# Optimization experiments

Measured on AMD Instinct MI355X. Metric: run time of the kernel, lower is better.

The kernel has to match this reference:

```python
import jax, jax.numpy as jnp
import numpy as np

B, C, H, W = 4, 512, 64, 64
INTER = 64  # C // channel_stride


def setup_inputs() -> dict:
    key = jax.random.key(0)
    ks = jax.random.split(key, 5)
    s = 0.02  # small init scale for numerical stability of softmax logits
    return {
        "inputs": jax.random.normal(ks[0], (B, C, H, W), dtype=jnp.float32),
        "Wq": jax.random.normal(ks[1], (INTER, C), dtype=jnp.float32) * s,
        "bq": jnp.zeros((INTER,), dtype=jnp.float32),
        "Wk": jax.random.normal(ks[2], (INTER, C), dtype=jnp.float32) * s,
        "bk": jnp.zeros((INTER,), dtype=jnp.float32),
        "Wv": jax.random.normal(ks[3], (C, C), dtype=jnp.float32) * s,
        "bv": jnp.zeros((C,), dtype=jnp.float32),
        "gamma": jax.random.normal(ks[4], (1,), dtype=jnp.float32),
    }


def reference(inputs, Wq, bq, Wk, bk, Wv, bv, gamma):
    b, c, h, w = inputs.shape
    n = h * w
    x = inputs.reshape(b, c, n)  # (B, C, N)
    # 1x1 convs == per-pixel linear projections
    q = jnp.einsum('dc,bcn->bnd', Wq, x) + bq            # (B, N, d)
    k = jnp.einsum('dc,bcn->bdn', Wk, x) + bk[:, None]   # (B, d, N)
    v = jnp.einsum('oc,bcn->bon', Wv, x) + bv[:, None]   # (B, O, N)
    # affinity: (B, Nq, Nk), softmax over keys (last dim), no scaling (as in source)
    affinity = jax.nn.softmax(jnp.einsum('bnd,bdm->bnm', q, k), axis=-1)
    # note: torch does bmm(value, affinity) -> out[b,o,m] = sum_j v[b,o,j] * A[b,j,m]
    out = jnp.einsum('bon,bnm->bom', v, affinity)        # (B, O, N)
    return gamma * out.reshape(b, -1, h, w) + inputs
```

## Files before the change

### kernel.cpp

```cpp
#include <hip/hip_runtime.h>
#include <stdint.h>

typedef __attribute__((ext_vector_type(8))) short short8;
typedef __attribute__((ext_vector_type(4))) float f32x4;
typedef __attribute__((ext_vector_type(8))) unsigned short u16x8;
typedef __attribute__((ext_vector_type(4))) unsigned short u16x4;
typedef __attribute__((ext_vector_type(2))) unsigned short u16x2;
typedef unsigned short u16;

#define NPIX 4096
#define CCH  512
#define DD   64

__device__ inline float b2f(u16 h){
  union { unsigned int i; float f; } u; u.i = ((unsigned int)h) << 16; return u.f;
}
__device__ inline u16 f2b(float f){
  union { float f; unsigned int i; } u; u.f = f;
  return (u16)((u.i + 0x7fffu + ((u.i >> 16) & 1u)) >> 16);
}
__device__ inline void gl2lds16(const void* g, void* l){
  __builtin_amdgcn_global_load_lds((const __attribute__((address_space(1))) unsigned int*)g,
                                   (__attribute__((address_space(3))) unsigned int*)l, 16, 0, 0);
}
__device__ inline f32x4 mfma16(short8 a, short8 b, f32x4 c){
  return __builtin_amdgcn_mfma_f32_16x16x32_bf16(a, b, c, 0, 0, 0);
}

__global__ __launch_bounds__(256) void k_cvt(const float* __restrict__ src,
                                             u16* __restrict__ dst, int n){
  int i = blockIdx.x * 256 + threadIdx.x;
  if (i < n) dst[i] = f2b(src[i]);
}

__global__ __launch_bounds__(256) void k0_transpose(const float* __restrict__ x,
                                                    u16* __restrict__ xT){
  __shared__ u16 tile[64][66];
  const int b = blockIdx.z;
  const int n0 = blockIdx.x * 64, c0 = blockIdx.y * 64;
  const float* xb = x + ((size_t)b * CCH + c0) * NPIX + n0;
  #pragma unroll
  for (int r = 0; r < 16; ++r){
    int id = r * 256 + threadIdx.x;
    int cc = id >> 6, nn = id & 63;
    tile[nn][cc] = f2b(xb[(size_t)cc * NPIX + nn]);
  }
  __syncthreads();
  u16* xTb = xT + ((size_t)b * NPIX + n0) * CCH + c0;
  #pragma unroll
  for (int r = 0; r < 8; ++r){
    int id = r * 256 + threadIdx.x;
    int nn = id >> 5, c2 = id & 31;
    *(u16x2*)(xTb + (size_t)nn * CCH + 2 * c2) = *(const u16x2*)&tile[nn][2 * c2];
  }
}

__global__ __launch_bounds__(256) void k1_qk(const u16* __restrict__ xT,
    const u16* __restrict__ Wqk, const float* __restrict__ bq,
    const float* __restrict__ bk, u16* __restrict__ Qb, u16* __restrict__ Kb){
  __shared__ __align__(16) u16 As[128*64];
  __shared__ __align__(16) u16 Bs[128*64];
  const int b  = blockIdx.z;
  const int n0 = blockIdx.x * 128;
  const u16* Ab = xT + ((size_t)b * NPIX + n0) * CCH;
  const int t = threadIdx.x, wave = t >> 6, lane = t & 63, q = lane >> 4, l16 = lane & 15;
  const int wr = (wave >> 1) * 64, wc = (wave & 1) * 64;
  f32x4 acc[4][4];
  #pragma unroll
  for (int i = 0; i < 4; ++i)
    #pragma unroll
    for (int j = 0; j < 4; ++j) acc[i][j] = (f32x4){0.f,0.f,0.f,0.f};

  for (int k0 = 0; k0 < CCH; k0 += 64){
    __syncthreads();
    #pragma unroll
    for (int r = 0; r < 4; ++r){
      int id = r * 256 + t;
      int row = id >> 3, ko = (id & 7) << 3;
      gl2lds16(Ab + (size_t)row * CCH + k0 + ko, &As[id * 8]);
      gl2lds16(Wqk + (size_t)row * CCH + k0 + ko, &Bs[id * 8]);
    }
    __syncthreads();
    #pragma unroll
    for (int s = 0; s < 2; ++s){
      short8 af[4], bfr[4];
      #pragma unroll
      for (int i = 0; i < 4; ++i){
        af[i]  = *(const short8*)&As[(wr + i*16 + l16)*64 + s*32 + q*8];
        bfr[i] = *(const short8*)&Bs[(wc + i*16 + l16)*64 + s*32 + q*8];
      }
      #pragma unroll
      for (int i = 0; i < 4; ++i)
        #pragma unroll
        for (int j = 0; j < 4; ++j)
          acc[i][j] = mfma16(af[i], bfr[j], acc[i][j]);
    }
  }
  #pragma unroll
  for (int i = 0; i < 4; ++i){
    #pragma unroll
    for (int j = 0; j < 4; ++j){
      int col = wc + j*16 + l16;
      #pragma unroll
      for (int r2 = 0; r2 < 4; ++r2){
        int n = n0 + wr + i*16 + q*4 + r2;
        float v = acc[i][j][r2];
        if (col < 64) Qb[((size_t)b * NPIX + n) * DD + col]        = f2b(v + bq[col]);
        else          Kb[((size_t)b * NPIX + n) * DD + (col - 64)] = f2b(v + bk[col - 64]);
      }
    }
  }
}

__global__ __launch_bounds__(256) void k2_v(const u16* __restrict__ xT,
    const u16* __restrict__ Wvb, const float* __restrict__ bv, u16* __restrict__ Vb){
  __shared__ __align__(16) u16 As[128*64];
  __shared__ __align__(16) u16 Bs[128*64];
  const int b  = blockIdx.z;
  const int n0 = blockIdx.x * 128;
  const int o0 = blockIdx.y * 128;
  const u16* Ab = Wvb + (size_t)o0 * CCH;
  const u16* Bb = xT + ((size_t)b * NPIX + n0) * CCH;
  const int t = threadIdx.x, wave = t >> 6, lane = t & 63, q = lane >> 4, l16 = lane & 15;
  const int wr = (wave >> 1) * 64, wc = (wave & 1) * 64;
  f32x4 acc[4][4];
  #pragma unroll
  for (int i = 0; i < 4; ++i)
    #pragma unroll
    for (int j = 0; j < 4; ++j) acc[i][j] = (f32x4){0.f,0.f,0.f,0.f};

  for (int k0 = 0; k0 < CCH; k0 += 64){
    __syncthreads();
    #pragma unroll
    for (int r = 0; r < 4; ++r){
      int id = r * 256 + t;
      int row = id >> 3, ko = (id & 7) << 3;
      gl2lds16(Ab + (size_t)row * CCH + k0 + ko, &As[id * 8]);
      gl2lds16(Bb + (size_t)row * CCH + k0 + ko, &Bs[id * 8]);
    }
    __syncthreads();
    #pragma unroll
    for (int s = 0; s < 2; ++s){
      short8 af[4], bfr[4];
      #pragma unroll
      for (int i = 0; i < 4; ++i){
        af[i]  = *(const short8*)&As[(wr + i*16 + l16)*64 + s*32 + q*8];
        bfr[i] = *(const short8*)&Bs[(wc + i*16 + l16)*64 + s*32 + q*8];
      }
      #pragma unroll
      for (int i = 0; i < 4; ++i)
        #pragma unroll
        for (int j = 0; j < 4; ++j)
          acc[i][j] = mfma16(af[i], bfr[j], acc[i][j]);
    }
  }
  #pragma unroll
  for (int i = 0; i < 4; ++i){
    #pragma unroll
    for (int j = 0; j < 4; ++j){
      int n = n0 + wc + j*16 + l16;
      #pragma unroll
      for (int r2 = 0; r2 < 4; ++r2){
        int o = o0 + wr + i*16 + q*4 + r2;
        Vb[((size_t)b * CCH + o) * NPIX + n] = f2b(acc[i][j][r2] + bv[o]);
      }
    }
  }
}

__global__ __launch_bounds__(256) void k3_logits(const u16* __restrict__ Qb,
    const u16* __restrict__ Kb, u16* __restrict__ E, float* __restrict__ Z, int b0){
  __shared__ __align__(16) u16 smem[128*136];
  u16* As = smem;
  u16* Bs = smem + 128*64;
  const int bloc = blockIdx.z, b = b0 + bloc;
  const int n0 = blockIdx.x * 128;
  const int m0 = blockIdx.y * 128;
  const u16* Ab = Kb + ((size_t)b * NPIX + m0) * DD;
  const u16* Bb = Qb + ((size_t)b * NPIX + n0) * DD;
  const int t = threadIdx.x, wave = t >> 6, lane = t & 63, q = lane >> 4, l16 = lane & 15;
  const int wr = (wave >> 1) * 64, wc = (wave & 1) * 64;
  f32x4 acc[4][4];
  #pragma unroll
  for (int i = 0; i < 4; ++i)
    #pragma unroll
    for (int j = 0; j < 4; ++j) acc[i][j] = (f32x4){0.f,0.f,0.f,0.f};

  #pragma unroll
  for (int r = 0; r < 4; ++r){
    int id = r * 256 + t;
    int row = id >> 3, ko = (id & 7) << 3;
    gl2lds16(Ab + row * DD + ko, &As[id * 8]);
    gl2lds16(Bb + row * DD + ko, &Bs[id * 8]);
  }
  __syncthreads();
  #pragma unroll
  for (int s = 0; s < 2; ++s){
    short8 af[4], bfr[4];
    #pragma unroll
    for (int i = 0; i < 4; ++i){
      af[i]  = *(const short8*)&As[(wr + i*16 + l16)*64 + s*32 + q*8];
      bfr[i] = *(const short8*)&Bs[(wc + i*16 + l16)*64 + s*32 + q*8];
    }
    #pragma unroll
    for (int i = 0; i < 4; ++i)
      #pragma unroll
      for (int j = 0; j < 4; ++j)
        acc[i][j] = mfma16(af[i], bfr[j], acc[i][j]);
  }
  __syncthreads();
  u16* tile = smem;
  float colsum[4] = {0.f, 0.f, 0.f, 0.f};
  #pragma unroll
  for (int i = 0; i < 4; ++i){
    #pragma unroll
    for (int j = 0; j < 4; ++j){
      #pragma unroll
      for (int r2 = 0; r2 < 4; ++r2){
        int mrow = wr + i*16 + q*4 + r2;
        int ncol = wc + j*16 + l16;
        float l = fminf(fmaxf(acc[i][j][r2], -60.f), 30.f);
        float e = __expf(l);
        tile[mrow * 136 + ncol] = f2b(e);
        colsum[j] += e;
      }
    }
  }
  #pragma unroll
  for (int j = 0; j < 4; ++j){
    float v = colsum[j];
    v += __shfl_xor(v, 16, 64);
    v += __shfl_xor(v, 32, 64);
    if (q == 0) atomicAdd(&Z[(size_t)b * NPIX + n0 + wc + j*16 + l16], v);
  }
  __syncthreads();
  u16* Eb = E + (size_t)bloc * NPIX * NPIX;
  #pragma unroll
  for (int r = 0; r < 8; ++r){
    int id = r * 256 + t;
    int row = id >> 4, chunk = id & 15;
    *(u16x8*)(Eb + (size_t)(m0 + row) * NPIX + n0 + chunk * 8) =
        *(const u16x8*)&tile[row * 136 + chunk * 8];
  }
}

__global__ __launch_bounds__(256) void k3b_scale(u16* __restrict__ Vb,
    const float* __restrict__ Z, const float* __restrict__ gm, int b0){
  size_t i4  = ((size_t)blockIdx.x * 256 + threadIdx.x) * 4;
  size_t off = ((size_t)b0 << 21) + i4;
  int b = (int)(off >> 21);
  int n = (int)(off & (NPIX - 1));
  float g = gm[0];
  u16x4 vv = *(const u16x4*)(Vb + off);
  f32x4 zz = *(const f32x4*)(Z + ((size_t)b << 12) + n);
  u16x4 r;
  #pragma unroll
  for (int k = 0; k < 4; ++k) r[k] = f2b(g * b2f(vv[k]) / fmaxf(zz[k], 1e-20f));
  *(u16x4*)(Vb + off) = r;
}

__global__ __launch_bounds__(256) void k4_out(const u16* __restrict__ Vs,
    const u16* __restrict__ E, const float* __restrict__ xin,
    float* __restrict__ outp, int b0){
  __shared__ __align__(16) u16 As[128*64];
  __shared__ __align__(16) u16 Bs[128*64];
  const int bloc = blockIdx.z, b = b0 + bloc;
  const int m0 = blockIdx.x * 128;
  const int o0 = blockIdx.y * 128;
  const u16* Ab = Vs + ((size_t)b * CCH + o0) * NPIX;
  const u16* Bb = E + (size_t)bloc * NPIX * NPIX + (size_t)m0 * NPIX;
  const int t = threadIdx.x, wave = t >> 6, lane = t & 63, q = lane >> 4, l16 = lane & 15;
  const int wr = (wave >> 1) * 64, wc = (wave & 1) * 64;
  f32x4 acc[4][4];
  #pragma unroll
  for (int i = 0; i < 4; ++i)
    #pragma unroll
    for (int j = 0; j < 4; ++j) acc[i][j] = (f32x4){0.f,0.f,0.f,0.f};

  for (int k0 = 0; k0 < NPIX; k0 += 64){
    __syncthreads();
    #pragma unroll
    for (int r = 0; r < 4; ++r){
      int id = r * 256 + t;
      int row = id >> 3, ko = (id & 7) << 3;
      gl2lds16(Ab + (size_t)row * NPIX + k0 + ko, &As[id * 8]);
      gl2lds16(Bb + (size_t)row * NPIX + k0 + ko, &Bs[id * 8]);
    }
    __syncthreads();
    #pragma unroll
    for (int s = 0; s < 2; ++s){
      short8 af[4], bfr[4];
      #pragma unroll
      for (int i = 0; i < 4; ++i){
        af[i]  = *(const short8*)&As[(wr + i*16 + l16)*64 + s*32 + q*8];
        bfr[i] = *(const short8*)&Bs[(wc + i*16 + l16)*64 + s*32 + q*8];
      }
      #pragma unroll
      for (int i = 0; i < 4; ++i)
        #pragma unroll
        for (int j = 0; j < 4; ++j)
          acc[i][j] = mfma16(af[i], bfr[j], acc[i][j]);
    }
  }
  const float* xb = xin + (size_t)b * CCH * NPIX;
  float* ob = outp + (size_t)b * CCH * NPIX;
  #pragma unroll
  for (int i = 0; i < 4; ++i){
    #pragma unroll
    for (int j = 0; j < 4; ++j){
      int m = m0 + wc + j*16 + l16;
      #pragma unroll
      for (int r2 = 0; r2 < 4; ++r2){
        int o = o0 + wr + i*16 + q*4 + r2;
        size_t idx = (size_t)o * NPIX + m;
        ob[idx] = acc[i][j][r2] + xb[idx];
      }
    }
  }
}

extern "C" void kernel_launch(void* const* d_in, const int* in_sizes, int n_in,
                              void* d_out, int out_size, void* d_ws, size_t ws_size,
                              hipStream_t stream){
  (void)in_sizes; (void)n_in; (void)out_size;
  const float* x  = (const float*)d_in[0];
  const float* Wq = (const float*)d_in[1];
  const float* bq = (const float*)d_in[2];
  const float* Wk = (const float*)d_in[3];
  const float* bk = (const float*)d_in[4];
  const float* Wv = (const float*)d_in[5];
  const float* bv = (const float*)d_in[6];
  const float* gm = (const float*)d_in[7];
  float* outp = (float*)d_out;

  char* ws = (char*)d_ws;
  u16*  Qb   = (u16*)(ws + 0);
  u16*  Kb   = (u16*)(ws + 2097152);
  u16*  Vb   = (u16*)(ws + 4194304);
  float* Z   = (float*)(ws + 20971520);
  u16*  Wqkb = (u16*)(ws + 21037056);
  u16*  Wvb  = (u16*)(ws + 21168128);
  u16*  xT   = (u16*)(ws + 21692416);
  u16*  E    = (u16*)(ws + 21692416);

  const size_t ebytes = (size_t)NPIX * NPIX * 2;
  const size_t base   = 21692416;
  if (ws_size < base + ebytes){
    return;
  }
  int NB = 1;
  if (ws_size >= base + 4 * ebytes) NB = 4;
  else if (ws_size >= base + 2 * ebytes) NB = 2;

  hipMemsetAsync(Z, 0, (size_t)4 * NPIX * sizeof(float), stream);
  k_cvt<<<dim3(128), 256, 0, stream>>>(Wq, Wqkb, 32768);
  k_cvt<<<dim3(128), 256, 0, stream>>>(Wk, Wqkb + 32768, 32768);
  k_cvt<<<dim3(1024), 256, 0, stream>>>(Wv, Wvb, 262144);
  k0_transpose<<<dim3(64, 8, 4), 256, 0, stream>>>(x, xT);
  k1_qk<<<dim3(32, 1, 4), 256, 0, stream>>>(xT, Wqkb, bq, bk, Qb, Kb);
  k2_v<<<dim3(32, 4, 4), 256, 0, stream>>>(xT, Wvb, bv, Vb);
  for (int b0 = 0; b0 < 4; b0 += NB){
    int nb = NB; if (b0 + nb > 4) nb = 4 - b0;
    k3_logits<<<dim3(32, 32, nb), 256, 0, stream>>>(Qb, Kb, E, Z, b0);
    k3b_scale<<<dim3(nb * 2048), 256, 0, stream>>>(Vb, Z, gm, b0);
    k4_out<<<dim3(32, 4, nb), 256, 0, stream>>>(Vb, E, x, outp, b0);
  }
}
```

Before: 262.8 us.

## Pre-swizzle global bf16 layouts so LDS fragment reads avoid bank conflicts

Every intermediate bf16 buffer (converted weights, transposed input, Q, K, V, and the exp-logit matrix E) is now written to global memory with an XOR swizzle on its 8-element column chunks keyed by row index. The direct global-to-LDS loads therefore land already swizzled, and each MFMA GEMM reads its fragments at the XOR-permuted chunk offset. This targets the LDS bank conflicts caused by 16 lanes reading the same column offset in rows of stride 128 bytes. It adds XOR index math in producers, consumers and the scaling kernel, and requires every writer and reader of these buffers to agree on the permutation.

```diff
diff --git a/kernel.cpp b/kernel.cpp
--- a/kernel.cpp
+++ b/kernel.cpp
@@ -12,6 +12,7 @@
 #define CCH  512
 #define DD   64
 
+
 __device__ inline float b2f(u16 h){
   union { unsigned int i; float f; } u; u.i = ((unsigned int)h) << 16; return u.f;
 }
@@ -30,7 +31,10 @@
 __global__ __launch_bounds__(256) void k_cvt(const float* __restrict__ src,
                                              u16* __restrict__ dst, int n){
   int i = blockIdx.x * 256 + threadIdx.x;
-  if (i < n) dst[i] = f2b(src[i]);
+  if (i < n){
+    int row = i >> 9, col = i & 511;
+    dst[(row << 9) + (col ^ ((row & 7) << 3))] = f2b(src[i]);
+  }
 }
 
 __global__ __launch_bounds__(256) void k0_transpose(const float* __restrict__ x,
@@ -51,7 +55,8 @@
   for (int r = 0; r < 8; ++r){
     int id = r * 256 + threadIdx.x;
     int nn = id >> 5, c2 = id & 31;
-    *(u16x2*)(xTb + (size_t)nn * CCH + 2 * c2) = *(const u16x2*)&tile[nn][2 * c2];
+    int colp = (2 * c2) ^ ((nn & 7) << 3);
+    *(u16x2*)(xTb + (size_t)nn * CCH + colp) = *(const u16x2*)&tile[nn][2 * c2];
   }
 }
 
@@ -65,6 +70,7 @@
   const u16* Ab = xT + ((size_t)b * NPIX + n0) * CCH;
   const int t = threadIdx.x, wave = t >> 6, lane = t & 63, q = lane >> 4, l16 = lane & 15;
   const int wr = (wave >> 1) * 64, wc = (wave & 1) * 64;
+  const int sw = l16 & 7;
   f32x4 acc[4][4];
   #pragma unroll
   for (int i = 0; i < 4; ++i)
@@ -83,11 +89,12 @@
     __syncthreads();
     #pragma unroll
     for (int s = 0; s < 2; ++s){
+      const int ca = ((s*4 + q) ^ sw) << 3;
       short8 af[4], bfr[4];
       #pragma unroll
       for (int i = 0; i < 4; ++i){
-        af[i]  = *(const short8*)&As[(wr + i*16 + l16)*64 + s*32 + q*8];
-        bfr[i] = *(const short8*)&Bs[(wc + i*16 + l16)*64 + s*32 + q*8];
+        af[i]  = *(const short8*)&As[(wr + i*16 + l16)*64 + ca];
+        bfr[i] = *(const short8*)&Bs[(wc + i*16 + l16)*64 + ca];
       }
       #pragma unroll
       for (int i = 0; i < 4; ++i)
@@ -104,9 +111,10 @@
       #pragma unroll
       for (int r2 = 0; r2 < 4; ++r2){
         int n = n0 + wr + i*16 + q*4 + r2;
+        int sw8 = (n & 7) << 3;
         float v = acc[i][j][r2];
-        if (col < 64) Qb[((size_t)b * NPIX + n) * DD + col]        = f2b(v + bq[col]);
-        else          Kb[((size_t)b * NPIX + n) * DD + (col - 64)] = f2b(v + bk[col - 64]);
+        if (col < 64) Qb[((size_t)b * NPIX + n) * DD + (col ^ sw8)]        = f2b(v + bq[col]);
+        else          Kb[((size_t)b * NPIX + n) * DD + ((col - 64) ^ sw8)] = f2b(v + bk[col - 64]);
       }
     }
   }
@@ -123,6 +131,7 @@
   const u16* Bb = xT + ((size_t)b * NPIX + n0) * CCH;
   const int t = threadIdx.x, wave = t >> 6, lane = t & 63, q = lane >> 4, l16 = lane & 15;
   const int wr = (wave >> 1) * 64, wc = (wave & 1) * 64;
+  const int sw = l16 & 7;
   f32x4 acc[4][4];
   #pragma unroll
   for (int i = 0; i < 4; ++i)
@@ -141,11 +150,12 @@
     __syncthreads();
     #pragma unroll
     for (int s = 0; s < 2; ++s){
+      const int ca = ((s*4 + q) ^ sw) << 3;
       short8 af[4], bfr[4];
       #pragma unroll
       for (int i = 0; i < 4; ++i){
-        af[i]  = *(const short8*)&As[(wr + i*16 + l16)*64 + s*32 + q*8];
-        bfr[i] = *(const short8*)&Bs[(wc + i*16 + l16)*64 + s*32 + q*8];
+        af[i]  = *(const short8*)&As[(wr + i*16 + l16)*64 + ca];
+        bfr[i] = *(const short8*)&Bs[(wc + i*16 + l16)*64 + ca];
       }
       #pragma unroll
       for (int i = 0; i < 4; ++i)
@@ -162,7 +172,8 @@
       #pragma unroll
       for (int r2 = 0; r2 < 4; ++r2){
         int o = o0 + wr + i*16 + q*4 + r2;
-        Vb[((size_t)b * CCH + o) * NPIX + n] = f2b(acc[i][j][r2] + bv[o]);
+        int np = n ^ ((o & 7) << 3);
+        Vb[((size_t)b * CCH + o) * NPIX + np] = f2b(acc[i][j][r2] + bv[o]);
       }
     }
   }
@@ -180,6 +191,7 @@
   const u16* Bb = Qb + ((size_t)b * NPIX + n0) * DD;
   const int t = threadIdx.x, wave = t >> 6, lane = t & 63, q = lane >> 4, l16 = lane & 15;
   const int wr = (wave >> 1) * 64, wc = (wave & 1) * 64;
+  const int sw = l16 & 7;
   f32x4 acc[4][4];
   #pragma unroll
   for (int i = 0; i < 4; ++i)
@@ -196,11 +208,12 @@
   __syncthreads();
   #pragma unroll
   for (int s = 0; s < 2; ++s){
+    const int ca = ((s*4 + q) ^ sw) << 3;
     short8 af[4], bfr[4];
     #pragma unroll
     for (int i = 0; i < 4; ++i){
-      af[i]  = *(const short8*)&As[(wr + i*16 + l16)*64 + s*32 + q*8];
-      bfr[i] = *(const short8*)&Bs[(wc + i*16 + l16)*64 + s*32 + q*8];
+      af[i]  = *(const short8*)&As[(wr + i*16 + l16)*64 + ca];
+      bfr[i] = *(const short8*)&Bs[(wc + i*16 + l16)*64 + ca];
     }
     #pragma unroll
     for (int i = 0; i < 4; ++i)
@@ -239,7 +252,9 @@
   for (int r = 0; r < 8; ++r){
     int id = r * 256 + t;
     int row = id >> 4, chunk = id & 15;
-    *(u16x8*)(Eb + (size_t)(m0 + row) * NPIX + n0 + chunk * 8) =
+    int g = chunk >> 3, c3 = chunk & 7;
+    int colp = g * 64 + ((c3 ^ (row & 7)) << 3);
+    *(u16x8*)(Eb + (size_t)(m0 + row) * NPIX + n0 + colp) =
         *(const u16x8*)&tile[row * 136 + chunk * 8];
   }
 }
@@ -249,10 +264,12 @@
   size_t i4  = ((size_t)blockIdx.x * 256 + threadIdx.x) * 4;
   size_t off = ((size_t)b0 << 21) + i4;
   int b = (int)(off >> 21);
-  int n = (int)(off & (NPIX - 1));
+  int o = (int)((off >> 12) & 511);
+  int np = (int)(off & (NPIX - 1));
+  int nl = np ^ ((o & 7) << 3);
   float g = gm[0];
   u16x4 vv = *(const u16x4*)(Vb + off);
-  f32x4 zz = *(const f32x4*)(Z + ((size_t)b << 12) + n);
+  f32x4 zz = *(const f32x4*)(Z + ((size_t)b << 12) + nl);
   u16x4 r;
   #pragma unroll
   for (int k = 0; k < 4; ++k) r[k] = f2b(g * b2f(vv[k]) / fmaxf(zz[k], 1e-20f));
@@ -271,6 +288,7 @@
   const u16* Bb = E + (size_t)bloc * NPIX * NPIX + (size_t)m0 * NPIX;
   const int t = threadIdx.x, wave = t >> 6, lane = t & 63, q = lane >> 4, l16 = lane & 15;
   const int wr = (wave >> 1) * 64, wc = (wave & 1) * 64;
+  const int sw = l16 & 7;
   f32x4 acc[4][4];
   #pragma unroll
   for (int i = 0; i < 4; ++i)
@@ -289,11 +307,12 @@
     __syncthreads();
     #pragma unroll
     for (int s = 0; s < 2; ++s){
+      const int ca = ((s*4 + q) ^ sw) << 3;
       short8 af[4], bfr[4];
       #pragma unroll
       for (int i = 0; i < 4; ++i){
-        af[i]  = *(const short8*)&As[(wr + i*16 + l16)*64 + s*32 + q*8];
-        bfr[i] = *(const short8*)&Bs[(wc + i*16 + l16)*64 + s*32 + q*8];
+        af[i]  = *(const short8*)&As[(wr + i*16 + l16)*64 + ca];
+        bfr[i] = *(const short8*)&Bs[(wc + i*16 + l16)*64 + ca];
       }
       #pragma unroll
       for (int i = 0; i < 4; ++i)
```

New measurement: 251.5 us. 4.3% less time.
